# Optimization experiments

Measured on AMD Instinct MI355X. Metric: run time of the kernel, lower is better.

Reference implementation:

```python
import jax, jax.numpy as jnp
import numpy as np

EPS = 1e-5

def conv1x1(x, w, b):
    # x: [B,C,H,W], w: [O,C], b: [O] -> [B,O,H,W]
    return jnp.einsum('bchw,oc->bohw', x, w) + b[None, :, None, None]

def batchnorm(x, gamma, beta):
    # training-mode BN over (N,H,W) with biased variance, matching torch forward
    mean = jnp.mean(x, axis=(0, 2, 3), keepdims=True)
    var = jnp.var(x, axis=(0, 2, 3), keepdims=True)
    xhat = (x - mean) * jax.lax.rsqrt(var + EPS)
    return xhat * gamma[None, :, None, None] + beta[None, :, None, None]

def setup_inputs() -> dict:
    key = jax.random.key(0)
    ks = jax.random.split(key, 16)
    B, C, F_int, H, W = 16, 256, 128, 64, 64
    s = 0.05
    return {
        'g': jax.random.normal(ks[0], (B, C, H, W), jnp.float32),
        'x': jax.random.normal(ks[1], (B, C, H, W), jnp.float32),
        'wg_w': jax.random.normal(ks[2], (F_int, C), jnp.float32) * s,
        'wg_b': jax.random.normal(ks[3], (F_int,), jnp.float32) * s,
        'wg_gamma': jnp.ones((F_int,), jnp.float32),
        'wg_beta': jnp.zeros((F_int,), jnp.float32),
        'wx_w': jax.random.normal(ks[4], (F_int, C), jnp.float32) * s,
        'wx_b': jax.random.normal(ks[5], (F_int,), jnp.float32) * s,
        'wx_gamma': jnp.ones((F_int,), jnp.float32),
        'wx_beta': jnp.zeros((F_int,), jnp.float32),
        'psi_w': jax.random.normal(ks[6], (1, F_int), jnp.float32) * s,
        'psi_b': jax.random.normal(ks[7], (1,), jnp.float32) * s,
        'psi_gamma': jnp.ones((1,), jnp.float32),
        'psi_beta': jnp.zeros((1,), jnp.float32),
    }

def reference(g, x, wg_w, wg_b, wg_gamma, wg_beta,
              wx_w, wx_b, wx_gamma, wx_beta,
              psi_w, psi_b, psi_gamma, psi_beta):
    g1 = batchnorm(conv1x1(g, wg_w, wg_b), wg_gamma, wg_beta)
    x1 = batchnorm(conv1x1(x, wx_w, wx_b), wx_gamma, wx_beta)
    psi = jax.nn.relu(g1 + x1)
    psi = jax.nn.sigmoid(batchnorm(conv1x1(psi, psi_w, psi_b), psi_gamma, psi_beta))
    return x * psi
```

## Files before the change

kernel.cpp:

```cpp
#include <hip/hip_runtime.h>
#include <hip/hip_bf16.h>
#include <math.h>

#define Bn 16
#define Cc 256
#define Oo 128
#define HWn 4096
#define Ntot 65536
#define BK 64
#define NBLK 512

typedef __attribute__((ext_vector_type(8))) __bf16 bf16x8;
typedef __attribute__((ext_vector_type(4))) float f32x4;

__device__ __forceinline__ unsigned short f2bf(float f) {
    unsigned u = __builtin_bit_cast(unsigned, f);
    u = (u + 0x7FFFu + ((u >> 16) & 1u)) >> 16;
    return (unsigned short)u;
}

__global__ __launch_bounds__(256, 2)
void conv_mfma(const float* __restrict__ gin, const float* __restrict__ xin,
               const float* __restrict__ wgw, const float* __restrict__ wgb,
               const float* __restrict__ wxw, const float* __restrict__ wxb,
               float* __restrict__ tg, float* __restrict__ tx,
               float* __restrict__ pstat)
{
    const int z = blockIdx.z;
    const float* in   = z ? xin : gin;
    const float* w    = z ? wxw : wgw;
    const float* bias = z ? wxb : wgb;
    float* out  = z ? tx : tg;

    __shared__ short A_s[128][72];
    __shared__ unsigned int B_s[32][129];

    const int t    = threadIdx.x;
    const int b    = blockIdx.y;
    const int hw0  = blockIdx.x * 128;
    const int lane = t & 63;
    const int wv   = t >> 6;
    const int m0   = (wv & 1) * 64;
    const int n0   = (wv >> 1) * 64;
    const int q    = lane >> 4;
    const int r    = lane & 15;

    const int su  = t & 31;
    const int sc2 = t >> 5;
    const int au  = t & 15;
    const int ao  = t >> 4;

    f32x4 acc[4][4];
#pragma unroll
    for (int i = 0; i < 4; i++)
#pragma unroll
        for (int j = 0; j < 4; j++) acc[i][j] = (f32x4){0.f, 0.f, 0.f, 0.f};

    float4 bv[8];
    float4 av[8];
    auto issue = [&](int kc) {
#pragma unroll
        for (int i = 0; i < 4; i++) {
            const int c = kc + (sc2 + i * 8) * 2;
            bv[2 * i + 0] = *(const float4*)(in + (b * Cc + c) * HWn + hw0 + su * 4);
            bv[2 * i + 1] = *(const float4*)(in + (b * Cc + c + 1) * HWn + hw0 + su * 4);
        }
#pragma unroll
        for (int i = 0; i < 8; i++)
            av[i] = *(const float4*)(w + (ao + i * 16) * Cc + kc + au * 4);
    };

    issue(0);

    for (int kc = 0; kc < Cc; kc += BK) {
#pragma unroll
        for (int i = 0; i < 4; i++) {
            const int c2 = sc2 + i * 8;
            const float4 v0 = bv[2 * i + 0];
            const float4 v1 = bv[2 * i + 1];
            uint4 pk;
            pk.x = (unsigned)f2bf(v0.x) | ((unsigned)f2bf(v1.x) << 16);
            pk.y = (unsigned)f2bf(v0.y) | ((unsigned)f2bf(v1.y) << 16);
            pk.z = (unsigned)f2bf(v0.z) | ((unsigned)f2bf(v1.z) << 16);
            pk.w = (unsigned)f2bf(v0.w) | ((unsigned)f2bf(v1.w) << 16);
            *(uint4*)&B_s[c2][su * 4] = pk;
        }
#pragma unroll
        for (int i = 0; i < 8; i++) {
            const int o = ao + i * 16;
            const float4 v = av[i];
            unsigned int lo = (unsigned)f2bf(v.x) | ((unsigned)f2bf(v.y) << 16);
            unsigned int hi = (unsigned)f2bf(v.z) | ((unsigned)f2bf(v.w) << 16);
            *(uint2*)&A_s[o][au * 4] = make_uint2(lo, hi);
        }
        __syncthreads();

        if (kc + BK < Cc) issue(kc + BK);

#pragma unroll
        for (int ks = 0; ks < 2; ks++) {
            bf16x8 af[4];
#pragma unroll
            for (int mi = 0; mi < 4; mi++)
                af[mi] = *(const bf16x8*)&A_s[m0 + mi * 16 + r][ks * 32 + q * 8];
#pragma unroll
            for (int ni = 0; ni < 4; ni++) {
                unsigned int bw[4];
                const int nn = n0 + ni * 16 + r;
                const int row = ks * 16 + q * 4;
#pragma unroll
                for (int jj = 0; jj < 4; jj++) bw[jj] = B_s[row + jj][nn];
                const bf16x8 bfr = *(const bf16x8*)bw;
#pragma unroll
                for (int mi = 0; mi < 4; mi++)
                    acc[mi][ni] = __builtin_amdgcn_mfma_f32_16x16x32_bf16(af[mi], bfr, acc[mi][ni], 0, 0, 0);
            }
        }
        __syncthreads();
    }

    float* red = (float*)&A_s[0][0];
    const int hf = wv >> 1;
#pragma unroll
    for (int mi = 0; mi < 4; mi++) {
#pragma unroll
        for (int reg = 0; reg < 4; reg++) {
            const int o = m0 + mi * 16 + q * 4 + reg;
            const float bo = bias[o];
            float s1 = 0.f, s2 = 0.f;
#pragma unroll
            for (int ni = 0; ni < 4; ni++) {
                const float v = acc[mi][ni][reg] + bo;
                out[((b * Oo + o) << 12) + hw0 + n0 + ni * 16 + r] = v;
                s1 += v; s2 += v * v;
            }
#pragma unroll
            for (int d = 1; d < 16; d <<= 1) {
                s1 += __shfl_xor(s1, d);
                s2 += __shfl_xor(s2, d);
            }
            if (r == 0) {
                red[(hf * 2 + 0) * 128 + o] = s1;
                red[(hf * 2 + 1) * 128 + o] = s2;
            }
        }
    }
    __syncthreads();
    {
        const int o = t & 127;
        const int s = t >> 7;
        const float v = red[(0 + s) * 128 + o] + red[(2 + s) * 128 + o];
        const int blk = blockIdx.y * 32 + blockIdx.x;
        pstat[(size_t)(((((z << 7) | o) << 1) | s) << 9) | blk] = v;
    }
}

__global__ void finalize1(const float* __restrict__ pstat,
                          const float* __restrict__ wg_gamma, const float* __restrict__ wg_beta,
                          const float* __restrict__ wx_gamma, const float* __restrict__ wx_beta,
                          const float* __restrict__ psi_w, float4* __restrict__ coef)
{
    const int t = threadIdx.x;
    const int z = t >> 7;
    const int o = t & 127;
    const float4* p1 = (const float4*)(pstat + (size_t)(((((z << 7) | o) << 1) | 0) << 9));
    const float4* p2 = (const float4*)(pstat + (size_t)(((((z << 7) | o) << 1) | 1) << 9));
    float s1 = 0.f, s2 = 0.f;
#pragma unroll 4
    for (int i = 0; i < 128; i++) {
        const float4 a = p1[i];
        const float4 c = p2[i];
        s1 += (a.x + a.y) + (a.z + a.w);
        s2 += (c.x + c.y) + (c.z + c.w);
    }
    const float invN = 1.f / (float)Ntot;
    const float m = s1 * invN;
    const float v = s2 * invN - m * m;
    const float sc = (z ? wx_gamma : wg_gamma)[o] * rsqrtf(v + 1e-5f);
    const float sh = (z ? wx_beta : wg_beta)[o] - m * sc;
    __shared__ float shsc[2][128], shsh[2][128];
    shsc[z][o] = sc; shsh[z][o] = sh;
    __syncthreads();
    if (t < 128)
        coef[t] = make_float4(shsc[0][t], shsc[1][t], shsh[0][t] + shsh[1][t], psi_w[t]);
}

__global__ __launch_bounds__(256)
void psi_partial(const float* __restrict__ tg, const float* __restrict__ tx,
                 const float4* __restrict__ coef, const float* __restrict__ psi_b,
                 float* __restrict__ S, float* __restrict__ pp)
{
    const int lane = threadIdx.x & 63;
    const int wv   = threadIdx.x >> 6;
    const int p    = blockIdx.x * 64 + lane;
    const int b    = p >> 12;
    const int hw   = p & 4095;
    const float* g0 = tg + (((size_t)(b * Oo + wv * 32)) << 12) + hw;
    const float* x0 = tx + (((size_t)(b * Oo + wv * 32)) << 12) + hw;
    float s = 0.f;
#pragma unroll
    for (int oi = 0; oi < 32; oi++) {
        const float4 cf = coef[wv * 32 + oi];
        const float gv = g0[(size_t)oi << 12];
        const float xv = x0[(size_t)oi << 12];
        s += cf.w * fmaxf(cf.x * gv + cf.y * xv + cf.z, 0.f);
    }
    __shared__ float sr[4][64];
    sr[wv][lane] = s;
    __syncthreads();
    if (wv == 0) {
        float st = s + sr[1][lane] + sr[2][lane] + sr[3][lane] + psi_b[0];
        S[p] = st;
        float s1 = st, s2 = st * st;
#pragma unroll
        for (int d = 1; d < 64; d <<= 1) {
            s1 += __shfl_xor(s1, d);
            s2 += __shfl_xor(s2, d);
        }
        if (lane == 0) {
            pp[blockIdx.x]        = s1;
            pp[1024 + blockIdx.x] = s2;
        }
    }
}

__global__ void finalize2(const float* __restrict__ pp, const float* __restrict__ psi_gamma,
                          const float* __restrict__ psi_beta, float* __restrict__ pc)
{
    const int t = threadIdx.x;
    float s1 = pp[t] + pp[256 + t] + pp[512 + t] + pp[768 + t];
    float s2 = pp[1024 + t] + pp[1280 + t] + pp[1536 + t] + pp[1792 + t];
#pragma unroll
    for (int d = 1; d < 64; d <<= 1) {
        s1 += __shfl_xor(s1, d);
        s2 += __shfl_xor(s2, d);
    }
    __shared__ float a1[4], a2[4];
    const int wid = t >> 6, lid = t & 63;
    if (lid == 0) { a1[wid] = s1; a2[wid] = s2; }
    __syncthreads();
    if (t == 0) {
        const float invN = 1.f / (float)Ntot;
        const float ts1 = a1[0] + a1[1] + a1[2] + a1[3];
        const float ts2 = a2[0] + a2[1] + a2[2] + a2[3];
        const float m = ts1 * invN;
        const float v = ts2 * invN - m * m;
        const float ps = psi_gamma[0] * rsqrtf(v + 1e-5f);
        pc[0] = ps;
        pc[1] = psi_beta[0] - m * ps;
    }
}

__global__ __launch_bounds__(256)
void final_mul_kernel(const float* __restrict__ x, const float* __restrict__ S,
                      const float* __restrict__ pc, float* __restrict__ out)
{
    const size_t i = ((size_t)blockIdx.x * 256 + threadIdx.x) * 4;
    const int hw = (int)(i & 4095);
    const size_t bc = i >> 12;
    const int b = (int)(bc >> 8);
    const float ps = pc[0], psh = pc[1];
    const float4 xv = *(const float4*)(x + i);
    const float4 sv = *(const float4*)(S + ((size_t)b << 12) + hw);
    float4 r;
    r.x = xv.x * (1.f / (1.f + __expf(-(ps * sv.x + psh))));
    r.y = xv.y * (1.f / (1.f + __expf(-(ps * sv.y + psh))));
    r.z = xv.z * (1.f / (1.f + __expf(-(ps * sv.z + psh))));
    r.w = xv.w * (1.f / (1.f + __expf(-(ps * sv.w + psh))));
    *(float4*)(out + i) = r;
}

extern "C" void kernel_launch(void* const* d_in, const int* in_sizes, int n_in,
                              void* d_out, int out_size, void* d_ws, size_t ws_size,
                              hipStream_t stream)
{
    const float* g         = (const float*)d_in[0];
    const float* x         = (const float*)d_in[1];
    const float* wg_w      = (const float*)d_in[2];
    const float* wg_b      = (const float*)d_in[3];
    const float* wg_gamma  = (const float*)d_in[4];
    const float* wg_beta   = (const float*)d_in[5];
    const float* wx_w      = (const float*)d_in[6];
    const float* wx_b      = (const float*)d_in[7];
    const float* wx_gamma  = (const float*)d_in[8];
    const float* wx_beta   = (const float*)d_in[9];
    const float* psi_w     = (const float*)d_in[10];
    const float* psi_b     = (const float*)d_in[11];
    const float* psi_gamma = (const float*)d_in[12];
    const float* psi_beta  = (const float*)d_in[13];

    float* out = (float*)d_out;
    float* tg = out;
    float* tx = out + (size_t)Bn * Oo * HWn;

    float* ws    = (float*)d_ws;
    float* S     = ws;
    float* pstat = ws + 65536;
    float* pp    = ws + 65536 + 262144;
    float4* coef = (float4*)(ws + 329728);
    float* pc    = ws + 330240;


    conv_mfma<<<dim3(HWn / 128, Bn, 2), 256, 0, stream>>>(
        g, x, wg_w, wg_b, wx_w, wx_b, tg, tx, pstat);
    finalize1<<<1, 256, 0, stream>>>(pstat, wg_gamma, wg_beta, wx_gamma, wx_beta,
                                     psi_w, coef);
    psi_partial<<<Ntot / 64, 256, 0, stream>>>(tg, tx, coef, psi_b, S, pp);
    finalize2<<<1, 256, 0, stream>>>(pp, psi_gamma, psi_beta, pc);
    final_mul_kernel<<<(Ntot * Cc) / (4 * 256), 256, 0, stream>>>(x, S, pc, out);
}
```

Baseline: 261.3 us.

## Store conv intermediates in bf16, drop BN-cancelled biases, parallelize stat reductions

```diff
diff --git a/kernel.cpp b/kernel.cpp
--- a/kernel.cpp
+++ b/kernel.cpp
@@ -8,7 +8,6 @@
 #define HWn 4096
 #define Ntot 65536
 #define BK 64
-#define NBLK 512
 
 typedef __attribute__((ext_vector_type(8))) __bf16 bf16x8;
 typedef __attribute__((ext_vector_type(4))) float f32x4;
@@ -19,18 +18,20 @@
     return (unsigned short)u;
 }
 
+__device__ __forceinline__ float bf2f(unsigned short h) {
+    return __builtin_bit_cast(float, (unsigned)h << 16);
+}
+
 __global__ __launch_bounds__(256, 2)
 void conv_mfma(const float* __restrict__ gin, const float* __restrict__ xin,
-               const float* __restrict__ wgw, const float* __restrict__ wgb,
-               const float* __restrict__ wxw, const float* __restrict__ wxb,
-               float* __restrict__ tg, float* __restrict__ tx,
+               const float* __restrict__ wgw, const float* __restrict__ wxw,
+               unsigned short* __restrict__ tg, unsigned short* __restrict__ tx,
                float* __restrict__ pstat)
 {
     const int z = blockIdx.z;
-    const float* in   = z ? xin : gin;
-    const float* w    = z ? wxw : wgw;
-    const float* bias = z ? wxb : wgb;
-    float* out  = z ? tx : tg;
+    const float* in = z ? xin : gin;
+    const float* w  = z ? wxw : wgw;
+    unsigned short* out = z ? tx : tg;
 
     __shared__ short A_s[128][72];
     __shared__ unsigned int B_s[32][129];
@@ -126,12 +127,11 @@
 #pragma unroll
         for (int reg = 0; reg < 4; reg++) {
             const int o = m0 + mi * 16 + q * 4 + reg;
-            const float bo = bias[o];
             float s1 = 0.f, s2 = 0.f;
 #pragma unroll
             for (int ni = 0; ni < 4; ni++) {
-                const float v = acc[mi][ni][reg] + bo;
-                out[((b * Oo + o) << 12) + hw0 + n0 + ni * 16 + r] = v;
+                const float v = acc[mi][ni][reg];
+                out[((b * Oo + o) << 12) + hw0 + n0 + ni * 16 + r] = f2bf(v);
                 s1 += v; s2 += v * v;
             }
 #pragma unroll
@@ -160,91 +160,106 @@
                           const float* __restrict__ wx_gamma, const float* __restrict__ wx_beta,
                           const float* __restrict__ psi_w, float4* __restrict__ coef)
 {
+    const int o = blockIdx.x;
     const int t = threadIdx.x;
-    const int z = t >> 7;
-    const int o = t & 127;
-    const float4* p1 = (const float4*)(pstat + (size_t)(((((z << 7) | o) << 1) | 0) << 9));
-    const float4* p2 = (const float4*)(pstat + (size_t)(((((z << 7) | o) << 1) | 1) << 9));
-    float s1 = 0.f, s2 = 0.f;
-#pragma unroll 4
-    for (int i = 0; i < 128; i++) {
-        const float4 a = p1[i];
-        const float4 c = p2[i];
-        s1 += (a.x + a.y) + (a.z + a.w);
-        s2 += (c.x + c.y) + (c.z + c.w);
-    }
-    const float invN = 1.f / (float)Ntot;
-    const float m = s1 * invN;
-    const float v = s2 * invN - m * m;
-    const float sc = (z ? wx_gamma : wg_gamma)[o] * rsqrtf(v + 1e-5f);
-    const float sh = (z ? wx_beta : wg_beta)[o] - m * sc;
-    __shared__ float shsc[2][128], shsh[2][128];
-    shsc[z][o] = sc; shsh[z][o] = sh;
-    __syncthreads();
-    if (t < 128)
-        coef[t] = make_float4(shsc[0][t], shsc[1][t], shsh[0][t] + shsh[1][t], psi_w[t]);
+    const float* r00 = pstat + (size_t)(((0 * 128 + o) * 2 + 0)) * 512;
+    const float* r01 = pstat + (size_t)(((0 * 128 + o) * 2 + 1)) * 512;
+    const float* r10 = pstat + (size_t)(((1 * 128 + o) * 2 + 0)) * 512;
+    const float* r11 = pstat + (size_t)(((1 * 128 + o) * 2 + 1)) * 512;
+    float s1g = r00[t] + r00[t + 256];
+    float s2g = r01[t] + r01[t + 256];
+    float s1x = r10[t] + r10[t + 256];
+    float s2x = r11[t] + r11[t + 256];
+#pragma unroll
+    for (int d = 1; d < 64; d <<= 1) {
+        s1g += __shfl_xor(s1g, d);
+        s2g += __shfl_xor(s2g, d);
+        s1x += __shfl_xor(s1x, d);
+        s2x += __shfl_xor(s2x, d);
+    }
+    __shared__ float rr[4][4];
+    const int wv = t >> 6, lid = t & 63;
+    if (lid == 0) { rr[0][wv] = s1g; rr[1][wv] = s2g; rr[2][wv] = s1x; rr[3][wv] = s2x; }
+    __syncthreads();
+    if (t == 0) {
+        const float invN = 1.f / (float)Ntot;
+        const float S1g = rr[0][0] + rr[0][1] + rr[0][2] + rr[0][3];
+        const float S2g = rr[1][0] + rr[1][1] + rr[1][2] + rr[1][3];
+        const float S1x = rr[2][0] + rr[2][1] + rr[2][2] + rr[2][3];
+        const float S2x = rr[3][0] + rr[3][1] + rr[3][2] + rr[3][3];
+        const float mg = S1g * invN;
+        const float vg = S2g * invN - mg * mg;
+        const float gs = wg_gamma[o] * rsqrtf(vg + 1e-5f);
+        const float gh = wg_beta[o] - mg * gs;
+        const float mx = S1x * invN;
+        const float vx = S2x * invN - mx * mx;
+        const float xs = wx_gamma[o] * rsqrtf(vx + 1e-5f);
+        const float xh = wx_beta[o] - mx * xs;
+        coef[o] = make_float4(gs, xs, gh + xh, psi_w[o]);
+    }
 }
 
 __global__ __launch_bounds__(256)
-void psi_partial(const float* __restrict__ tg, const float* __restrict__ tx,
-                 const float4* __restrict__ coef, const float* __restrict__ psi_b,
-                 float* __restrict__ S, float* __restrict__ pp)
-{
-    const int lane = threadIdx.x & 63;
-    const int wv   = threadIdx.x >> 6;
-    const int p    = blockIdx.x * 64 + lane;
-    const int b    = p >> 12;
-    const int hw   = p & 4095;
-    const float* g0 = tg + (((size_t)(b * Oo + wv * 32)) << 12) + hw;
-    const float* x0 = tx + (((size_t)(b * Oo + wv * 32)) << 12) + hw;
+void psi_k(const unsigned short* __restrict__ tg, const unsigned short* __restrict__ tx,
+           const float4* __restrict__ coef, float* __restrict__ S, float* __restrict__ pp)
+{
+    __shared__ float4 cf[128];
+    const int t = threadIdx.x;
+    if (t < 128) cf[t] = coef[t];
+    __syncthreads();
+
+    const int p  = blockIdx.x * 256 + t;
+    const int b  = p >> 12;
+    const int hw = p & 4095;
+    const unsigned short* gp = tg + (((size_t)(b * Oo)) << 12) + hw;
+    const unsigned short* xp = tx + (((size_t)(b * Oo)) << 12) + hw;
     float s = 0.f;
-#pragma unroll
-    for (int oi = 0; oi < 32; oi++) {
-        const float4 cf = coef[wv * 32 + oi];
-        const float gv = g0[(size_t)oi << 12];
-        const float xv = x0[(size_t)oi << 12];
-        s += cf.w * fmaxf(cf.x * gv + cf.y * xv + cf.z, 0.f);
-    }
-    __shared__ float sr[4][64];
-    sr[wv][lane] = s;
-    __syncthreads();
-    if (wv == 0) {
-        float st = s + sr[1][lane] + sr[2][lane] + sr[3][lane] + psi_b[0];
-        S[p] = st;
-        float s1 = st, s2 = st * st;
-#pragma unroll
-        for (int d = 1; d < 64; d <<= 1) {
-            s1 += __shfl_xor(s1, d);
-            s2 += __shfl_xor(s2, d);
-        }
-        if (lane == 0) {
-            pp[blockIdx.x]        = s1;
-            pp[1024 + blockIdx.x] = s2;
-        }
-    }
-}
-
-__global__ void finalize2(const float* __restrict__ pp, const float* __restrict__ psi_gamma,
-                          const float* __restrict__ psi_beta, float* __restrict__ pc)
-{
-    const int t = threadIdx.x;
-    float s1 = pp[t] + pp[256 + t] + pp[512 + t] + pp[768 + t];
-    float s2 = pp[1024 + t] + pp[1280 + t] + pp[1536 + t] + pp[1792 + t];
+#pragma unroll 16
+    for (int o = 0; o < 128; o++) {
+        const float gv = bf2f(gp[(size_t)o << 12]);
+        const float xv = bf2f(xp[(size_t)o << 12]);
+        const float4 c = cf[o];
+        s += c.w * fmaxf(c.x * gv + c.y * xv + c.z, 0.f);
+    }
+    S[p] = s;
+
+    float s1 = s, s2 = s * s;
 #pragma unroll
     for (int d = 1; d < 64; d <<= 1) {
         s1 += __shfl_xor(s1, d);
         s2 += __shfl_xor(s2, d);
     }
+    __shared__ float r1[4], r2[4];
+    const int wv = t >> 6, lid = t & 63;
+    if (lid == 0) { r1[wv] = s1; r2[wv] = s2; }
+    __syncthreads();
+    if (t == 0) {
+        pp[blockIdx.x]       = r1[0] + r1[1] + r1[2] + r1[3];
+        pp[256 + blockIdx.x] = r2[0] + r2[1] + r2[2] + r2[3];
+    }
+}
+
+__global__ void finalize2(const float* __restrict__ pp, const float* __restrict__ psi_gamma,
+                          const float* __restrict__ psi_beta, float* __restrict__ pc)
+{
+    const int t = threadIdx.x;
+    float s1 = pp[t];
+    float s2 = pp[256 + t];
+#pragma unroll
+    for (int d = 1; d < 64; d <<= 1) {
+        s1 += __shfl_xor(s1, d);
+        s2 += __shfl_xor(s2, d);
+    }
     __shared__ float a1[4], a2[4];
     const int wid = t >> 6, lid = t & 63;
     if (lid == 0) { a1[wid] = s1; a2[wid] = s2; }
     __syncthreads();
     if (t == 0) {
         const float invN = 1.f / (float)Ntot;
-        const float ts1 = a1[0] + a1[1] + a1[2] + a1[3];
-        const float ts2 = a2[0] + a2[1] + a2[2] + a2[3];
-        const float m = ts1 * invN;
-        const float v = ts2 * invN - m * m;
+        const float S1 = a1[0] + a1[1] + a1[2] + a1[3];
+        const float S2 = a2[0] + a2[1] + a2[2] + a2[3];
+        const float m = S1 * invN;
+        const float v = S2 * invN - m * m;
         const float ps = psi_gamma[0] * rsqrtf(v + 1e-5f);
         pc[0] = ps;
         pc[1] = psi_beta[0] - m * ps;
@@ -277,35 +292,32 @@
     const float* g         = (const float*)d_in[0];
     const float* x         = (const float*)d_in[1];
     const float* wg_w      = (const float*)d_in[2];
-    const float* wg_b      = (const float*)d_in[3];
     const float* wg_gamma  = (const float*)d_in[4];
     const float* wg_beta   = (const float*)d_in[5];
     const float* wx_w      = (const float*)d_in[6];
-    const float* wx_b      = (const float*)d_in[7];
     const float* wx_gamma  = (const float*)d_in[8];
     const float* wx_beta   = (const float*)d_in[9];
     const float* psi_w     = (const float*)d_in[10];
-    const float* psi_b     = (const float*)d_in[11];
     const float* psi_gamma = (const float*)d_in[12];
     const float* psi_beta  = (const float*)d_in[13];
 
     float* out = (float*)d_out;
-    float* tg = out;
-    float* tx = out + (size_t)Bn * Oo * HWn;
+    unsigned short* tg = (unsigned short*)out;
+    unsigned short* tx = (unsigned short*)out + (size_t)Bn * Oo * HWn;
 
     float* ws    = (float*)d_ws;
     float* S     = ws;
     float* pstat = ws + 65536;
-    float* pp    = ws + 65536 + 262144;
-    float4* coef = (float4*)(ws + 329728);
-    float* pc    = ws + 330240;
+    float4* coef = (float4*)(ws + 327680);
+    float* pp    = ws + 327680 + 512;
+    float* pc    = ws + 328704;
 
 
     conv_mfma<<<dim3(HWn / 128, Bn, 2), 256, 0, stream>>>(
-        g, x, wg_w, wg_b, wx_w, wx_b, tg, tx, pstat);
-    finalize1<<<1, 256, 0, stream>>>(pstat, wg_gamma, wg_beta, wx_gamma, wx_beta,
-                                     psi_w, coef);
-    psi_partial<<<Ntot / 64, 256, 0, stream>>>(tg, tx, coef, psi_b, S, pp);
+        g, x, wg_w, wx_w, tg, tx, pstat);
+    finalize1<<<128, 256, 0, stream>>>(pstat, wg_gamma, wg_beta, wx_gamma, wx_beta,
+                                       psi_w, coef);
+    psi_k<<<256, 256, 0, stream>>>(tg, tx, coef, S, pp);
     finalize2<<<1, 256, 0, stream>>>(pp, psi_gamma, psi_beta, pc);
     final_mul_kernel<<<(Ntot * Cc) / (4 * 256), 256, 0, stream>>>(x, S, pc, out);
 }
```

New measurement: 257.2 us. No clear change (-1.5%).
